# Kernel tuning notes

Hardware: AMD Instinct MI355X
Metric: run time of the kernel (lower is better)

Reference implementation:

```python
import jax, jax.numpy as jnp
import numpy as np

V_PATCH_NUMS = (1, 2, 4, 6, 8, 10, 13, 16)
HW = 16
QUANT_RESI = 0.5
SHARE_K = 4
BETA = 1.0


def _pool_matrix(n_in, n_out):
    # adaptive average pooling as a [n_out, n_in] matrix (matches F.adaptive_avg_pool2d bins)
    P = np.zeros((n_out, n_in), np.float32)
    for i in range(n_out):
        s = (i * n_in) // n_out
        e = -((-(i + 1) * n_in) // n_out)  # ceil((i+1)*n_in/n_out)
        P[i, s:e] = 1.0 / (e - s)
    return jnp.asarray(P)


def _phi_index(si, SN):
    # PhiPartiallyShared.__getitem__(si/(SN-1)) with K=4 ticks
    K = SHARE_K
    ticks = np.linspace(1.0 / 3 / K, 1 - 1.0 / 3 / K, K) if K == 4 else np.linspace(1.0 / 2 / K, 1 - 1.0 / 2 / K, K)
    return int(np.argmin(np.abs(ticks - si / (SN - 1))))


def _phi(h, w, b):
    # Phi: h*(1-r) + conv3x3(h)*r, zero padding (nn.Conv2d default)
    y = jax.lax.conv_general_dilated(h, w, (1, 1), 'SAME',
                                     dimension_numbers=('NCHW', 'OIHW', 'NCHW'))
    y = y + b[None, :, None, None]
    return h * (1.0 - QUANT_RESI) + y * QUANT_RESI


def setup_inputs() -> dict:
    key = jax.random.key(0)
    k0, k1, k2 = jax.random.split(key, 3)
    B, C, V = 64, 32, 4096
    f = jax.random.normal(k0, (B, C, HW, HW), jnp.float32)
    embed = jax.random.normal(k1, (V, C), jnp.float32)  # EMAEmbedding.weight ~ randn
    phi_w = jax.random.normal(k2, (SHARE_K, C, C, 3, 3), jnp.float32) * (1.0 / np.sqrt(9.0 * C))
    phi_b = jnp.zeros((SHARE_K, C), jnp.float32)
    return {"f_BChw": f, "embed_weight": embed, "phi_w": phi_w, "phi_b": phi_b}


def reference(f_BChw, embed_weight, phi_w, phi_b):
    B, C, H, W = f_BChw.shape
    SN = len(V_PATCH_NUMS)
    f_ng = jax.lax.stop_gradient(f_BChw)
    f_hat = jnp.zeros_like(f_BChw)
    e_sq = jnp.sum(embed_weight * embed_weight, axis=1)  # [V]
    loss = jnp.float32(0.0)
    for si, pn in enumerate(V_PATCH_NUMS):
        rest = f_ng - jax.lax.stop_gradient(f_hat)  # residual to quantize (no grad through distance)
        if pn != H:
            P = _pool_matrix(H, pn)
            rest_d = jnp.einsum('oh,bchw,pw->bcop', P, rest, P)  # adaptive avg pool -> [B,C,pn,pn]
        else:
            rest_d = rest
        rest_NC = rest_d.transpose(0, 2, 3, 1).reshape(-1, C)  # [B*pn*pn, C]
        # squared euclidean cdist to codebook, argmin
        d = (jnp.sum(rest_NC * rest_NC, axis=1, keepdims=True)
             + e_sq[None, :]
             - 2.0 * (rest_NC @ embed_weight.T))  # [N, V]
        idx = jnp.argmin(d, axis=1)  # [B*pn*pn] int
        h = embed_weight[idx].reshape(B, pn, pn, C).transpose(0, 3, 1, 2)  # gather -> [B,C,pn,pn]
        if pn != H:
            h = jax.image.resize(h, (B, C, H, W), method='linear')  # bilinear, align_corners=False
        k = _phi_index(si, SN)
        h = _phi(h, phi_w[k], phi_b[k])
        f_hat = f_hat + h
        loss = loss + 0.25 * jnp.mean((jax.lax.stop_gradient(f_hat) - f_BChw) ** 2) \
                    + BETA * jnp.mean((f_hat - f_ng) ** 2)
    loss = loss / SN
    # straight-through estimator: grads flow to f_BChw as identity
    f_hat_st = jax.lax.stop_gradient(f_hat - f_BChw) + f_BChw
    return f_hat_st, loss
```

## Files before the change

### kernel.cpp

```cpp
#include <hip/hip_runtime.h>
#include <hip/hip_bf16.h>

#define BB 64
#define CC 32
#define HW2 256
#define VV 4096
#define NELEM (BB*CC*HW2)
#define NPAD 16640

#define OFF_F     0
#define OFF_FHAT  (OFF_F     + NELEM)
#define OFF_EMB   (OFF_FHAT  + NELEM)
#define OFF_ESQ   (OFF_EMB   + VV*CC)
#define OFF_PW    (OFF_ESQ   + VV)
#define OFF_PB    (OFF_PW    + 4*CC*CC*9)
#define OFF_REST  (OFF_PB    + 4*CC)
#define OFF_BESTA (OFF_REST  + CC*NPAD)
#define OFF_BESTB (OFF_BESTA + 2*NPAD)
#define OFF_LOSS  (OFF_BESTB + 2*NPAD)
#define OFF_FLAG  (OFF_LOSS  + 1)

__global__ void k_probe(const void* __restrict__ fin, int* __restrict__ flag) {
    __shared__ int cnt[256];
    int t = threadIdx.x;
    const __hip_bfloat16* p = (const __hip_bfloat16*)fin;
    int local = 0;
    for (int i = t; i < 8192; i += 256) {
        float v = __bfloat162float(p[i]);
        if (!(fabsf(v) < 1e3f)) local++;
    }
    cnt[t] = local;
    __syncthreads();
    for (int s = 128; s > 0; s >>= 1) {
        if (t < s) cnt[t] += cnt[t + s];
        __syncthreads();
    }
    if (t == 0) *flag = (cnt[0] >= 64) ? 1 : 0;
}

__global__ void k_prep(const void* __restrict__ fin,
                       const void* __restrict__ ein,
                       const void* __restrict__ win,
                       const void* __restrict__ bin_,
                       const int* __restrict__ flag,
                       float* __restrict__ f, float* __restrict__ fhat,
                       float* __restrict__ emb, float* __restrict__ pw,
                       float* __restrict__ pb, float* __restrict__ loss) {
    bool isf32 = (*flag != 0);
    int i = blockIdx.x * 256 + threadIdx.x;
    if (i < NELEM) {
        f[i] = isf32 ? ((const float*)fin)[i]
                     : __bfloat162float(((const __hip_bfloat16*)fin)[i]);
        fhat[i] = 0.f;
    }
    if (i < VV*CC)
        emb[i] = isf32 ? ((const float*)ein)[i]
                       : __bfloat162float(((const __hip_bfloat16*)ein)[i]);
    if (i < 4*CC*CC*9)
        pw[i] = isf32 ? ((const float*)win)[i]
                      : __bfloat162float(((const __hip_bfloat16*)win)[i]);
    if (i < 4*CC)
        pb[i] = isf32 ? ((const float*)bin_)[i]
                      : __bfloat162float(((const __hip_bfloat16*)bin_)[i]);
    if (i == 0) *loss = 0.f;
}

__global__ void k_esq(const float* __restrict__ emb, float* __restrict__ esq) {
    int v = blockIdx.x * 256 + threadIdx.x;
    if (v >= VV) return;
    const float* e = emb + v * CC;
    float s = 0.f;
    #pragma unroll
    for (int c = 0; c < CC; ++c) s = fmaf(e[c], e[c], s);
    esq[v] = s;
}

__global__ void k_pool0(const float* __restrict__ f, const float* __restrict__ fhat,
                        float* __restrict__ rest_t, unsigned long long* __restrict__ best) {
    int n = threadIdx.x;
    int c = blockIdx.y;
    if (n >= BB) return;
    if (c == 0) best[n] = 0xFFFFFFFFFFFFFFFFull;
    const float* fb = f + (n * CC + c) * HW2;
    const float* hb = fhat + (n * CC + c) * HW2;
    float s = 0.f;
    for (int h = 0; h < 16; ++h)
        for (int w = 0; w < 16; ++w)
            s += fb[h * 16 + w] - hb[h * 16 + w];
    rest_t[c * NPAD + n] = s * (1.f / 256.f);
}

__global__ __launch_bounds__(256, 1)
void k_argmin(const float* __restrict__ rest_t, const float* __restrict__ emb,
              const float* __restrict__ esq, unsigned long long* __restrict__ best,
              int Ntot, int cpw) {
    int n = blockIdx.x * 256 + threadIdx.x;
    bool valid = (n < Ntot);
    int nc = valid ? n : 0;
    int v0 = blockIdx.y * cpw;

    float xx = 0.f;
    #pragma unroll
    for (int c = 0; c < CC; ++c) {
        float xv = rest_t[c * NPAD + nc];
        xx = fmaf(xv, xv, xx);
    }

    float bd = 3.4e38f;
    int bi = v0;

    for (int vt = v0; vt < v0 + cpw; vt += 32) {
        float dacc[32];
        #pragma unroll
        for (int vi = 0; vi < 32; ++vi) dacc[vi] = 0.f;

        #pragma unroll
        for (int ct = 0; ct < CC; ct += 8) {
            float xc[8];
            #pragma unroll
            for (int c = 0; c < 8; ++c) xc[c] = rest_t[(ct + c) * NPAD + nc];
            #pragma unroll
            for (int vi = 0; vi < 32; ++vi) {
                const float* e = emb + (vt + vi) * CC + ct;
                #pragma unroll
                for (int c = 0; c < 8; ++c)
                    dacc[vi] = fmaf(xc[c], e[c], dacc[vi]);
            }
        }

        #pragma unroll
        for (int vi = 0; vi < 32; ++vi) {
            float dist = fmaf(-2.f, dacc[vi], xx + esq[vt + vi]);
            if (dist < bd) { bd = dist; bi = vt + vi; }
        }
    }

    if (valid) {
        unsigned u = __float_as_uint(bd);
        unsigned long long mono = (u & 0x80000000u)
            ? (unsigned long long)(~u)
            : (unsigned long long)(u | 0x80000000u);
        atomicMin(best + n, (mono << 32) | (unsigned long long)(unsigned)bi);
    }
}

__global__ __launch_bounds__(512)
void k_fuse(const float* __restrict__ emb,
            const unsigned long long* __restrict__ best,
            const float* __restrict__ pw, const float* __restrict__ pb,
            const float* __restrict__ f, float* __restrict__ fhat,
            float* __restrict__ loss,
            float* __restrict__ rest_t,
            unsigned long long* __restrict__ best_next,
            int pn, int k, int pn_next) {
    __shared__ float h_up[CC][HW2];
    __shared__ float extra[CC * 169];
    __shared__ float red[8];
    int b = blockIdx.x, coq = blockIdx.y, t = threadIdx.x;
    int nn = pn * pn;
    int pix = t & 255, half = t >> 8;
    int y = pix >> 4, x = pix & 15;
    int c0 = half * 16;

    if (pn == 16) {
        int id = (int)(unsigned)(best[b * HW2 + pix] & 0xFFFFFFFFull);
        const float* er = emb + id * CC + c0;
        #pragma unroll
        for (int c = 0; c < 16; ++c) h_up[c0 + c][pix] = er[c];
    } else {
        float (*hs)[169] = (float(*)[169])extra;
        for (int cell = t; cell < nn; cell += 512) {
            int id = (int)(unsigned)(best[b * nn + cell] & 0xFFFFFFFFull);
            const float* er = emb + id * CC;
            #pragma unroll
            for (int c = 0; c < CC; ++c) hs[c][cell] = er[c];
        }
        __syncthreads();
        float scale = (float)pn / 16.f;
        float sy = (y + 0.5f) * scale - 0.5f;
        sy = fminf(fmaxf(sy, 0.f), (float)(pn - 1));
        int y0 = (int)sy; int y1 = min(y0 + 1, pn - 1); float wy = sy - (float)y0;
        float sx = (x + 0.5f) * scale - 0.5f;
        sx = fminf(fmaxf(sx, 0.f), (float)(pn - 1));
        int x0 = (int)sx; int x1 = min(x0 + 1, pn - 1); float wx = sx - (float)x0;
        float wy0 = 1.f - wy, wx0 = 1.f - wx;
        #pragma unroll
        for (int c = 0; c < 16; ++c) {
            int cc = c0 + c;
            float v00 = hs[cc][y0 * pn + x0], v01 = hs[cc][y0 * pn + x1];
            float v10 = hs[cc][y1 * pn + x0], v11 = hs[cc][y1 * pn + x1];
            float a0 = wy0 * v00 + wy * v10;
            float a1 = wy0 * v01 + wy * v11;
            h_up[cc][pix] = wx0 * a0 + wx * a1;
        }
    }
    __syncthreads();

    float acc[4];
    #pragma unroll
    for (int o = 0; o < 4; ++o) acc[o] = 0.f;
    for (int ci_ = 0; ci_ < CC; ++ci_) {
        float hv[9];
        #pragma unroll
        for (int dy = 0; dy < 3; ++dy)
            #pragma unroll
            for (int dx = 0; dx < 3; ++dx) {
                int yy = y + dy - 1, xx2 = x + dx - 1;
                hv[dy * 3 + dx] = (yy >= 0 && yy < 16 && xx2 >= 0 && xx2 < 16)
                                  ? h_up[ci_][yy * 16 + xx2] : 0.f;
            }
        const float* wp = pw + ((k * CC + coq * 8 + half * 4) * CC + ci_) * 9;
        #pragma unroll
        for (int o = 0; o < 4; ++o) {
            const float* w9 = wp + o * (CC * 9);
            #pragma unroll
            for (int q = 0; q < 9; ++q) acc[o] = fmaf(hv[q], w9[q], acc[o]);
        }
    }

    float* diff = extra;
    float lsum = 0.f;
    #pragma unroll
    for (int o = 0; o < 4; ++o) {
        int lo = half * 4 + o;
        int co = coq * 8 + lo;
        float hval = h_up[co][pix];
        float outv = hval * 0.5f + (acc[o] + pb[k * CC + co]) * 0.5f;
        int pos = (b * CC + co) * HW2 + pix;
        float fh = fhat[pos] + outv;
        fhat[pos] = fh;
        float dd = f[pos] - fh;
        diff[lo * HW2 + pix] = dd;
        lsum = fmaf(dd, dd, lsum);
    }
    #pragma unroll
    for (int off = 32; off > 0; off >>= 1) lsum += __shfl_down(lsum, off, 64);
    if ((t & 63) == 0) red[t >> 6] = lsum;
    __syncthreads();
    if (t == 0) {
        float s = 0.f;
        #pragma unroll
        for (int w = 0; w < 8; ++w) s += red[w];
        atomicAdd(loss, s);
    }

    if (pn_next > 0) {
        int nn2 = pn_next * pn_next;
        for (int q = t; q < nn2 * 8; q += 512) {
            int cell = q % nn2, o = q / nn2;
            int i = cell / pn_next, j = cell % pn_next;
            int s0 = (i * 16) / pn_next, e0 = ((i + 1) * 16 + pn_next - 1) / pn_next;
            int s1 = (j * 16) / pn_next, e1 = ((j + 1) * 16 + pn_next - 1) / pn_next;
            float inv = 1.f / (float)((e0 - s0) * (e1 - s1));
            float s = 0.f;
            for (int h = s0; h < e0; ++h)
                for (int w = s1; w < e1; ++w)
                    s += diff[o * HW2 + h * 16 + w];
            rest_t[(coq * 8 + o) * NPAD + b * nn2 + cell] = s * inv;
        }
        if (coq == 0)
            for (int q = t; q < nn2; q += 512)
                best_next[b * nn2 + q] = 0xFFFFFFFFFFFFFFFFull;
    }
}

__global__ void k_out(const float* __restrict__ fhat, const float* __restrict__ loss,
                      const int* __restrict__ flag, void* __restrict__ out) {
    bool isf32 = (*flag != 0);
    int i = blockIdx.x * 256 + threadIdx.x;
    if (i > NELEM) return;
    float v;
    if (i < NELEM) v = fhat[i];
    else           v = (*loss) * (1.25f / (float)NELEM / 8.f);
    if (isf32) ((float*)out)[i] = v;
    else       ((__hip_bfloat16*)out)[i] = __float2bfloat16(v);
}

extern "C" void kernel_launch(void* const* d_in, const int* in_sizes, int n_in,
                              void* d_out, int out_size, void* d_ws, size_t ws_size,
                              hipStream_t stream) {
    const void* fin  = d_in[0];
    const void* ein  = d_in[1];
    const void* win  = d_in[2];
    const void* bin_ = d_in[3];
    float* ws = (float*)d_ws;
    float* f    = ws + OFF_F;
    float* fhat = ws + OFF_FHAT;
    float* emb  = ws + OFF_EMB;
    float* esq  = ws + OFF_ESQ;
    float* pw   = ws + OFF_PW;
    float* pb   = ws + OFF_PB;
    float* rest_t = ws + OFF_REST;
    unsigned long long* bestA = (unsigned long long*)(ws + OFF_BESTA);
    unsigned long long* bestB = (unsigned long long*)(ws + OFF_BESTB);
    float* loss = ws + OFF_LOSS;
    int*   flag = (int*)(ws + OFF_FLAG);

    static const int PN[8] = {1, 2, 4, 6, 8, 10, 13, 16};
    static const int KK[8] = {0, 0, 1, 1, 2, 2, 3, 3};
    static const int SP[8] = {128, 128, 128, 128, 128, 64, 64, 32};

    k_probe<<<1, 256, 0, stream>>>(fin, flag);
    k_prep<<<(NELEM + 255) / 256, 256, 0, stream>>>(fin, ein, win, bin_, flag, f, fhat, emb, pw, pb, loss);
    k_esq<<<(VV + 255) / 256, 256, 0, stream>>>(emb, esq);
    k_pool0<<<dim3(1, CC), 256, 0, stream>>>(f, fhat, rest_t, bestA);

    for (int si = 0; si < 8; ++si) {
        int pn = PN[si];
        int Ntot = BB * pn * pn;
        int Sp = SP[si];
        int cpw = VV / Sp;
        unsigned long long* bcur = (si & 1) ? bestB : bestA;
        unsigned long long* bnxt = (si & 1) ? bestA : bestB;
        int pn_next = (si < 7) ? PN[si + 1] : 0;
        int gx = (Ntot + 255) / 256;
        k_argmin<<<dim3(gx, Sp), 256, 0, stream>>>(rest_t, emb, esq, bcur, Ntot, cpw);
        k_fuse<<<dim3(BB, 4), 512, 0, stream>>>(emb, bcur, pw, pb, f, fhat, loss,
                                                rest_t, bnxt, pn, KK[si], pn_next);
    }
    k_out<<<(NELEM + 1 + 255) / 256, 256, 0, stream>>>(fhat, loss, flag, d_out);
}
```

Before: 549.7 us.

## Remap argmin so lanes span codes and waves share query rows

The codebook is stored in a tiled transposed layout (64 codes by 32 channels per tile), and residuals move to row-major [N,C]. The argmin kernel now gives each lane one code and each wave four query rows. Query values are wave-uniform, so they can be scalar or broadcast loads. Each lane keeps four running minima, which are reduced with 64-lane shuffles before a single atomicMin per query. The split counts over the codebook are retuned so each stage has enough blocks. The intent is to replace per-thread redundant codebook reads and large register arrays with coalesced code loads, at the cost of extra shuffle reductions.

```diff
diff --git a/kernel.cpp b/kernel.cpp
--- a/kernel.cpp
+++ b/kernel.cpp
@@ -6,19 +6,22 @@
 #define HW2 256
 #define VV 4096
 #define NELEM (BB*CC*HW2)
-#define NPAD 16640
 
 #define OFF_F     0
 #define OFF_FHAT  (OFF_F     + NELEM)
-#define OFF_EMB   (OFF_FHAT  + NELEM)
-#define OFF_ESQ   (OFF_EMB   + VV*CC)
+#define OFF_EMBT  (OFF_FHAT  + NELEM)
+#define OFF_ESQ   (OFF_EMBT  + VV*CC)
 #define OFF_PW    (OFF_ESQ   + VV)
 #define OFF_PB    (OFF_PW    + 4*CC*CC*9)
 #define OFF_REST  (OFF_PB    + 4*CC)
-#define OFF_BESTA (OFF_REST  + CC*NPAD)
-#define OFF_BESTB (OFF_BESTA + 2*NPAD)
-#define OFF_LOSS  (OFF_BESTB + 2*NPAD)
+#define OFF_BESTA (OFF_REST  + 16384*CC)
+#define OFF_BESTB (OFF_BESTA + 2*16384)
+#define OFF_LOSS  (OFF_BESTB + 2*16384)
 #define OFF_FLAG  (OFF_LOSS  + 1)
+
+__device__ __forceinline__ int embt_idx(int v, int c) {
+    return (v >> 6) * 2048 + c * 64 + (v & 63);
+}
 
 __global__ void k_probe(const void* __restrict__ fin, int* __restrict__ flag) {
     __shared__ int cnt[256];
@@ -44,7 +47,7 @@
                        const void* __restrict__ bin_,
                        const int* __restrict__ flag,
                        float* __restrict__ f, float* __restrict__ fhat,
-                       float* __restrict__ emb, float* __restrict__ pw,
+                       float* __restrict__ embT, float* __restrict__ pw,
                        float* __restrict__ pb, float* __restrict__ loss) {
     bool isf32 = (*flag != 0);
     int i = blockIdx.x * 256 + threadIdx.x;
@@ -53,9 +56,12 @@
                      : __bfloat162float(((const __hip_bfloat16*)fin)[i]);
         fhat[i] = 0.f;
     }
-    if (i < VV*CC)
-        emb[i] = isf32 ? ((const float*)ein)[i]
-                       : __bfloat162float(((const __hip_bfloat16*)ein)[i]);
+    if (i < VV*CC) {
+        float ev = isf32 ? ((const float*)ein)[i]
+                         : __bfloat162float(((const __hip_bfloat16*)ein)[i]);
+        int v = i >> 5, c = i & 31;
+        embT[embt_idx(v, c)] = ev;
+    }
     if (i < 4*CC*CC*9)
         pw[i] = isf32 ? ((const float*)win)[i]
                       : __bfloat162float(((const __hip_bfloat16*)win)[i]);
@@ -65,18 +71,18 @@
     if (i == 0) *loss = 0.f;
 }
 
-__global__ void k_esq(const float* __restrict__ emb, float* __restrict__ esq) {
+__global__ void k_esq(const float* __restrict__ embT, float* __restrict__ esq) {
     int v = blockIdx.x * 256 + threadIdx.x;
     if (v >= VV) return;
-    const float* e = emb + v * CC;
+    const float* p = embT + (v >> 6) * 2048 + (v & 63);
     float s = 0.f;
     #pragma unroll
-    for (int c = 0; c < CC; ++c) s = fmaf(e[c], e[c], s);
+    for (int c = 0; c < CC; ++c) { float e = p[c * 64]; s = fmaf(e, e, s); }
     esq[v] = s;
 }
 
 __global__ void k_pool0(const float* __restrict__ f, const float* __restrict__ fhat,
-                        float* __restrict__ rest_t, unsigned long long* __restrict__ best) {
+                        float* __restrict__ rest, unsigned long long* __restrict__ best) {
     int n = threadIdx.x;
     int c = blockIdx.y;
     if (n >= BB) return;
@@ -87,70 +93,90 @@
     for (int h = 0; h < 16; ++h)
         for (int w = 0; w < 16; ++w)
             s += fb[h * 16 + w] - hb[h * 16 + w];
-    rest_t[c * NPAD + n] = s * (1.f / 256.f);
-}
-
-__global__ __launch_bounds__(256, 1)
-void k_argmin(const float* __restrict__ rest_t, const float* __restrict__ emb,
+    rest[n * CC + c] = s * (1.f / 256.f);
+}
+
+__global__ __launch_bounds__(256)
+void k_argmin(const float* __restrict__ rest, const float* __restrict__ embT,
               const float* __restrict__ esq, unsigned long long* __restrict__ best,
               int Ntot, int cpw) {
-    int n = blockIdx.x * 256 + threadIdx.x;
-    bool valid = (n < Ntot);
-    int nc = valid ? n : 0;
+    int lane = threadIdx.x & 63;
+    int wave = threadIdx.x >> 6;
     int v0 = blockIdx.y * cpw;
-
-    float xx = 0.f;
-    #pragma unroll
-    for (int c = 0; c < CC; ++c) {
-        float xv = rest_t[c * NPAD + nc];
-        xx = fmaf(xv, xv, xx);
-    }
-
-    float bd = 3.4e38f;
-    int bi = v0;
-
-    for (int vt = v0; vt < v0 + cpw; vt += 32) {
-        float dacc[32];
-        #pragma unroll
-        for (int vi = 0; vi < 32; ++vi) dacc[vi] = 0.f;
-
-        #pragma unroll
-        for (int ct = 0; ct < CC; ct += 8) {
-            float xc[8];
-            #pragma unroll
-            for (int c = 0; c < 8; ++c) xc[c] = rest_t[(ct + c) * NPAD + nc];
-            #pragma unroll
-            for (int vi = 0; vi < 32; ++vi) {
-                const float* e = emb + (vt + vi) * CC + ct;
-                #pragma unroll
-                for (int c = 0; c < 8; ++c)
-                    dacc[vi] = fmaf(xc[c], e[c], dacc[vi]);
+    int t0 = v0 >> 6;
+    int qbase = __builtin_amdgcn_readfirstlane(blockIdx.x * 16 + wave * 4);
+
+    const float* xrp[4];
+    float xx[4];
+    #pragma unroll
+    for (int q = 0; q < 4; ++q) {
+        int nq = qbase + q; if (nq > Ntot - 1) nq = Ntot - 1;
+        xrp[q] = rest + nq * CC;
+        float s = 0.f;
+        #pragma unroll
+        for (int c = 0; c < CC; ++c) { float xv = xrp[q][c]; s = fmaf(xv, xv, s); }
+        xx[q] = s;
+    }
+
+    float bd[4]; int bi[4];
+    #pragma unroll
+    for (int q = 0; q < 4; ++q) { bd[q] = 3.4e38f; bi[q] = v0; }
+
+    int ntiles = cpw >> 6;
+    for (int t = 0; t < ntiles; ++t) {
+        const float* ep = embT + (size_t)(t0 + t) * 2048 + lane;
+        float es = esq[v0 + t * 64 + lane];
+        float da0 = 0.f, da1 = 0.f, da2 = 0.f, da3 = 0.f;
+        #pragma unroll
+        for (int cb = 0; cb < 4; ++cb) {
+            float e[8];
+            #pragma unroll
+            for (int i = 0; i < 8; ++i) e[i] = ep[(cb * 8 + i) * 64];
+            const float* x0 = xrp[0] + cb * 8;
+            const float* x1 = xrp[1] + cb * 8;
+            const float* x2 = xrp[2] + cb * 8;
+            const float* x3 = xrp[3] + cb * 8;
+            #pragma unroll
+            for (int i = 0; i < 8; ++i) {
+                da0 = fmaf(x0[i], e[i], da0);
+                da1 = fmaf(x1[i], e[i], da1);
+                da2 = fmaf(x2[i], e[i], da2);
+                da3 = fmaf(x3[i], e[i], da3);
             }
         }
-
-        #pragma unroll
-        for (int vi = 0; vi < 32; ++vi) {
-            float dist = fmaf(-2.f, dacc[vi], xx + esq[vt + vi]);
-            if (dist < bd) { bd = dist; bi = vt + vi; }
-        }
-    }
-
-    if (valid) {
-        unsigned u = __float_as_uint(bd);
+        float da[4] = {da0, da1, da2, da3};
+        int vcode = v0 + t * 64 + lane;
+        #pragma unroll
+        for (int q = 0; q < 4; ++q) {
+            float dist = fmaf(-2.f, da[q], xx[q] + es);
+            if (dist < bd[q]) { bd[q] = dist; bi[q] = vcode; }
+        }
+    }
+
+    #pragma unroll
+    for (int q = 0; q < 4; ++q) {
+        unsigned u = __float_as_uint(bd[q]);
         unsigned long long mono = (u & 0x80000000u)
             ? (unsigned long long)(~u)
             : (unsigned long long)(u | 0x80000000u);
-        atomicMin(best + n, (mono << 32) | (unsigned long long)(unsigned)bi);
+        unsigned long long pk = (mono << 32) | (unsigned long long)(unsigned)bi[q];
+        #pragma unroll
+        for (int off = 32; off > 0; off >>= 1) {
+            unsigned long long o = __shfl_down(pk, off, 64);
+            if (o < pk) pk = o;
+        }
+        if (lane == 0 && qbase + q < Ntot)
+            atomicMin(best + qbase + q, pk);
     }
 }
 
 __global__ __launch_bounds__(512)
-void k_fuse(const float* __restrict__ emb,
+void k_fuse(const float* __restrict__ embT,
             const unsigned long long* __restrict__ best,
             const float* __restrict__ pw, const float* __restrict__ pb,
             const float* __restrict__ f, float* __restrict__ fhat,
             float* __restrict__ loss,
-            float* __restrict__ rest_t,
+            float* __restrict__ rest,
             unsigned long long* __restrict__ best_next,
             int pn, int k, int pn_next) {
     __shared__ float h_up[CC][HW2];
@@ -164,16 +190,16 @@
 
     if (pn == 16) {
         int id = (int)(unsigned)(best[b * HW2 + pix] & 0xFFFFFFFFull);
-        const float* er = emb + id * CC + c0;
-        #pragma unroll
-        for (int c = 0; c < 16; ++c) h_up[c0 + c][pix] = er[c];
+        const float* er = embT + (id >> 6) * 2048 + (id & 63);
+        #pragma unroll
+        for (int c = 0; c < 16; ++c) h_up[c0 + c][pix] = er[(c0 + c) * 64];
     } else {
         float (*hs)[169] = (float(*)[169])extra;
         for (int cell = t; cell < nn; cell += 512) {
             int id = (int)(unsigned)(best[b * nn + cell] & 0xFFFFFFFFull);
-            const float* er = emb + id * CC;
-            #pragma unroll
-            for (int c = 0; c < CC; ++c) hs[c][cell] = er[c];
+            const float* er = embT + (id >> 6) * 2048 + (id & 63);
+            #pragma unroll
+            for (int c = 0; c < CC; ++c) hs[c][cell] = er[c * 64];
         }
         __syncthreads();
         float scale = (float)pn / 16.f;
@@ -256,7 +282,7 @@
             for (int h = s0; h < e0; ++h)
                 for (int w = s1; w < e1; ++w)
                     s += diff[o * HW2 + h * 16 + w];
-            rest_t[(coq * 8 + o) * NPAD + b * nn2 + cell] = s * inv;
+            rest[(b * nn2 + cell) * CC + coq * 8 + o] = s * inv;
         }
         if (coq == 0)
             for (int q = t; q < nn2; q += 512)
@@ -286,11 +312,11 @@
     float* ws = (float*)d_ws;
     float* f    = ws + OFF_F;
     float* fhat = ws + OFF_FHAT;
-    float* emb  = ws + OFF_EMB;
+    float* embT = ws + OFF_EMBT;
     float* esq  = ws + OFF_ESQ;
     float* pw   = ws + OFF_PW;
     float* pb   = ws + OFF_PB;
-    float* rest_t = ws + OFF_REST;
+    float* rest = ws + OFF_REST;
     unsigned long long* bestA = (unsigned long long*)(ws + OFF_BESTA);
     unsigned long long* bestB = (unsigned long long*)(ws + OFF_BESTB);
     float* loss = ws + OFF_LOSS;
@@ -298,12 +324,12 @@
 
     static const int PN[8] = {1, 2, 4, 6, 8, 10, 13, 16};
     static const int KK[8] = {0, 0, 1, 1, 2, 2, 3, 3};
-    static const int SP[8] = {128, 128, 128, 128, 128, 64, 64, 32};
+    static const int SP[8] = {64, 32, 8, 4, 2, 2, 1, 1};
 
     k_probe<<<1, 256, 0, stream>>>(fin, flag);
-    k_prep<<<(NELEM + 255) / 256, 256, 0, stream>>>(fin, ein, win, bin_, flag, f, fhat, emb, pw, pb, loss);
-    k_esq<<<(VV + 255) / 256, 256, 0, stream>>>(emb, esq);
-    k_pool0<<<dim3(1, CC), 256, 0, stream>>>(f, fhat, rest_t, bestA);
+    k_prep<<<(NELEM + 255) / 256, 256, 0, stream>>>(fin, ein, win, bin_, flag, f, fhat, embT, pw, pb, loss);
+    k_esq<<<(VV + 255) / 256, 256, 0, stream>>>(embT, esq);
+    k_pool0<<<dim3(1, CC), 256, 0, stream>>>(f, fhat, rest, bestA);
 
     for (int si = 0; si < 8; ++si) {
         int pn = PN[si];
@@ -313,10 +339,10 @@
         unsigned long long* bcur = (si & 1) ? bestB : bestA;
         unsigned long long* bnxt = (si & 1) ? bestA : bestB;
         int pn_next = (si < 7) ? PN[si + 1] : 0;
-        int gx = (Ntot + 255) / 256;
-        k_argmin<<<dim3(gx, Sp), 256, 0, stream>>>(rest_t, emb, esq, bcur, Ntot, cpw);
-        k_fuse<<<dim3(BB, 4), 512, 0, stream>>>(emb, bcur, pw, pb, f, fhat, loss,
-                                                rest_t, bnxt, pn, KK[si], pn_next);
+        int gx = (Ntot + 15) / 16;
+        k_argmin<<<dim3(gx, Sp), 256, 0, stream>>>(rest, embT, esq, bcur, Ntot, cpw);
+        k_fuse<<<dim3(BB, 4), 512, 0, stream>>>(embT, bcur, pw, pb, f, fhat, loss,
+                                                rest, bnxt, pn, KK[si], pn_next);
     }
     k_out<<<(NELEM + 1 + 255) / 256, 256, 0, stream>>>(fhat, loss, flag, d_out);
 }
```

After: 625.3 us. 1.14x slower.
